# Performance work log

Hardware: AMD Instinct MI355X
Metric: run time of the kernel (lower is better)

Reference implementation:

```python
import jax, jax.numpy as jnp
import numpy as np

EPS = 1e-8
LN_EPS = 1e-5

def _layernorm(x, g, b):
    mu = jnp.mean(x, axis=-1, keepdims=True)
    var = jnp.mean((x - mu) ** 2, axis=-1, keepdims=True)
    return (x - mu) / jnp.sqrt(var + LN_EPS) * g + b

def setup_inputs() -> dict:
    key = jax.random.key(0)
    ks = jax.random.split(key, 10)
    B, S = 8192, 4096
    input_dim, hidden_dim = 4, 256
    h4 = hidden_dim // 4  # 64
    price_series = jax.random.uniform(ks[0], (B, S, 1), dtype=jnp.float32) + 0.5
    # 4 parallel encoders stacked on leading axis: Linear(input_dim->h4) + LayerNorm(h4)
    enc_w = jax.random.normal(ks[1], (4, input_dim, h4), dtype=jnp.float32) * 0.5
    enc_b = jax.random.normal(ks[2], (4, h4), dtype=jnp.float32) * 0.02
    enc_g = jnp.ones((4, h4), dtype=jnp.float32)
    enc_beta = jnp.zeros((4, h4), dtype=jnp.float32)
    # regime head: Linear(hidden_dim->64) + ReLU + (Dropout eval=identity) + Linear(64->4)
    head_w1 = jax.random.normal(ks[3], (hidden_dim, 64), dtype=jnp.float32) * 0.0625
    head_b1 = jnp.zeros((64,), dtype=jnp.float32)
    head_w2 = jax.random.normal(ks[4], (64, 4), dtype=jnp.float32) * 0.125
    head_b2 = jnp.zeros((4,), dtype=jnp.float32)
    return {"price_series": price_series, "enc_w": enc_w, "enc_b": enc_b,
            "enc_g": enc_g, "enc_beta": enc_beta,
            "head_w1": head_w1, "head_b1": head_b1,
            "head_w2": head_w2, "head_b2": head_b2}

def reference(price_series, enc_w, enc_b, enc_g, enc_beta, head_w1, head_b1, head_w2, head_b2):
    prices = price_series[:, :, 0]  # [B, S]
    B, S = prices.shape
    # Rolling SMA(20) with clamped window start, via cumsum (single pass, no per-step loop)
    csum = jnp.concatenate([jnp.zeros((B, 1), prices.dtype), jnp.cumsum(prices, axis=1)], axis=1)  # [B, S+1]
    i = jnp.arange(S)
    start20 = jnp.maximum(0, i - 19)
    cnt20 = (i - start20 + 1).astype(prices.dtype)
    sma20 = (csum[:, i + 1] - csum[:, start20]) / cnt20  # [B, S]
    trend_signal = (prices - sma20) / (sma20 + EPS)
    f_trend = jnp.mean(trend_signal, axis=1, keepdims=True)  # [B,1]
    # momentum over last 10 steps
    p_last = prices[:, -1:]
    p_m10 = prices[:, -10:-9]
    f_mom = (p_last - p_m10) / (p_m10 + EPS)  # [B,1]
    # mean reversion
    p_mean = jnp.mean(prices, axis=1, keepdims=True)
    f_mr = (p_last - p_mean) / (p_mean + EPS)  # [B,1]
    # cycle: coefficient of variation (torch.std is unbiased, ddof=1)
    f_cyc = jnp.std(prices, axis=1, ddof=1, keepdims=True) / (p_mean + EPS)  # [B,1]
    combined = jnp.concatenate([f_trend, f_mom, f_mr, f_cyc], axis=1)  # [B, 4]
    # 4 parallel encoders: Linear -> ReLU -> LayerNorm
    pre = jnp.einsum('bi,eio->ebo', combined, enc_w) + enc_b[:, None, :]  # [4, B, 64]
    feats = _layernorm(jax.nn.relu(pre), enc_g[:, None, :], enc_beta[:, None, :])  # [4, B, 64]
    # concat order: trend, momentum, mean_rev, cycle along feature dim
    regime_features = jnp.transpose(feats, (1, 0, 2)).reshape(B, -1)  # [B, 256]
    h = jax.nn.relu(regime_features @ head_w1 + head_b1)
    regime_probs = jax.nn.softmax(h @ head_w2 + head_b2, axis=1)  # [B, 4]
    return (regime_features, regime_probs)
```

## Files before the change

kernel.cpp:

```cpp
#include <hip/hip_runtime.h>

#define EPS 1e-8f
#define LN_EPS 1e-5f
#define NROWS 8192
#define SLEN 4096
#define PROBS_OFF 2097152

typedef __attribute__((ext_vector_type(8))) short bf16x8;
typedef __attribute__((ext_vector_type(4))) float f32x4;

__device__ __forceinline__ short f2bf(float f) {
    unsigned u = __float_as_uint(f);
    unsigned r = (u + 0x7FFFu + ((u >> 16) & 1u)) >> 16;
    return (short)r;
}

#define SLP(i) ((i) + ((((i) >> 4)) << 2))

__global__ __launch_bounds__(256) void k_feat(const float* __restrict__ prices,
                                              float* __restrict__ ws) {
    __shared__ float sld[5156];
    __shared__ float red[4][3];

    const int t = threadIdx.x;
    const int b = blockIdx.x;
    const int lane = t & 63, wv = t >> 6;
    const float4* R4 = (const float4*)(prices + (size_t)b * SLEN);

    if (t < 8) *(float4*)&sld[SLP(4 * t)] = make_float4(0.f, 0.f, 0.f, 0.f);
    {
        float4 g0 = R4[t];
        float4 g1 = R4[t + 256];
        float4 g2 = R4[t + 512];
        float4 g3 = R4[t + 768];
        *(float4*)&sld[SLP(4 * (t + 8))]   = g0;
        *(float4*)&sld[SLP(4 * (t + 264))] = g1;
        *(float4*)&sld[SLP(4 * (t + 520))] = g2;
        *(float4*)&sld[SLP(4 * (t + 776))] = g3;
    }
    __syncthreads();

    const int e0 = 16 * t + 32;
    float4 s0 = *(const float4*)&sld[SLP(e0)];
    float4 s1 = *(const float4*)&sld[SLP(e0 + 4)];
    float4 s2 = *(const float4*)&sld[SLP(e0 + 8)];
    float4 s3 = *(const float4*)&sld[SLP(e0 + 12)];
    float4 q0 = *(const float4*)&sld[SLP(e0 - 20)];
    float4 q1 = *(const float4*)&sld[SLP(e0 - 16)];
    float4 q2 = *(const float4*)&sld[SLP(e0 - 12)];
    float4 q3 = *(const float4*)&sld[SLP(e0 - 8)];
    float4 q4 = *(const float4*)&sld[SLP(e0 - 4)];

    float xv[16] = { s0.x, s0.y, s0.z, s0.w, s1.x, s1.y, s1.z, s1.w,
                     s2.x, s2.y, s2.z, s2.w, s3.x, s3.y, s3.z, s3.w };
    float ov[16] = { q0.x, q0.y, q0.z, q0.w, q1.x, q1.y, q1.z, q1.w,
                     q2.x, q2.y, q2.z, q2.w, q3.x, q3.y, q3.z, q3.w };

    float W = q0.y + q0.z + q0.w
            + q1.x + q1.y + q1.z + q1.w
            + q2.x + q2.y + q2.z + q2.w
            + q3.x + q3.y + q3.z + q3.w
            + q4.x + q4.y + q4.z + q4.w;

    const float pf = (float)(16 * t);
    float sum = 0.0f, sq = 0.0f, ts = 0.0f;
    #pragma unroll
    for (int j = 0; j < 16; ++j) {
        float x = xv[j];
        W += (j == 0) ? x : (x - ov[j]);
        sum += x;
        sq = fmaf(x, x, sq);
        float c = fminf(pf + (float)(j + 1), 20.0f);
        float num = fmaf(x, c, -W);
        float den = fmaf(EPS, c, W);
        ts += num * __builtin_amdgcn_rcpf(den);
    }

    #pragma unroll
    for (int off = 32; off > 0; off >>= 1) {
        sum += __shfl_xor(sum, off);
        sq  += __shfl_xor(sq,  off);
        ts  += __shfl_xor(ts,  off);
    }
    if (lane == 0) { red[wv][0] = sum; red[wv][1] = sq; red[wv][2] = ts; }
    __syncthreads();

    if (t == 255) {
        float S = red[0][0] + red[1][0] + red[2][0] + red[3][0];
        float Q = red[0][1] + red[1][1] + red[2][1] + red[3][1];
        float T = red[0][2] + red[1][2] + red[2][2] + red[3][2];
        float mean = S * (1.0f / 4096.0f);
        float var  = fmaxf((Q - 4096.0f * mean * mean) * (1.0f / 4095.0f), 0.0f);
        float p_m10 = s1.z, p_last = s3.w;
        float4 f;
        f.x = T * (1.0f / 4096.0f);
        f.y = (p_last - p_m10) / (p_m10 + EPS);
        f.z = (p_last - mean) / (mean + EPS);
        f.w = sqrtf(var) / (mean + EPS);
        ((float4*)ws)[b] = f;
    }
}

#define ROWS 16

__global__ __launch_bounds__(256) void k_head(
    const float* __restrict__ ws, float* __restrict__ out,
    const float* __restrict__ enc_w, const float* __restrict__ enc_b,
    const float* __restrict__ enc_g, const float* __restrict__ enc_bt,
    const float* __restrict__ w1, const float* __restrict__ b1,
    const float* __restrict__ w2, const float* __restrict__ b2)
{
    __shared__ float comb[ROWS][4];
    __shared__ short rfb[ROWS][264];
    __shared__ float hbuf[ROWS][68];

    const int t = threadIdx.x;
    const int r0 = blockIdx.x * ROWS;
    const int lane = t & 63, wave = t >> 6;
    const int l15 = lane & 15, q = lane >> 4;

    if (t < ROWS) *(float4*)comb[t] = ((const float4*)ws)[r0 + t];

    bf16x8 bfrag[8];
    #pragma unroll
    for (int kt = 0; kt < 8; ++kt) {
        #pragma unroll
        for (int j = 0; j < 8; ++j) {
            int k = kt * 32 + q * 8 + j;
            bfrag[kt][j] = f2bf(w1[k * 64 + wave * 16 + l15]);
        }
    }

    const float ew0 = enc_w[wave * 256 + lane];
    const float ew1v = enc_w[wave * 256 + 64 + lane];
    const float ew2v = enc_w[wave * 256 + 128 + lane];
    const float ew3v = enc_w[wave * 256 + 192 + lane];
    const float ebv = enc_b[t], egv = enc_g[t], btv = enc_bt[t];

    __syncthreads();

    for (int r = 0; r < ROWS; r += 2) {
        float4 cba = *(const float4*)comb[r];
        float4 cbb = *(const float4*)comb[r + 1];
        float va = fmaf(cba.x, ew0, fmaf(cba.y, ew1v, fmaf(cba.z, ew2v, fmaf(cba.w, ew3v, ebv))));
        float vb = fmaf(cbb.x, ew0, fmaf(cbb.y, ew1v, fmaf(cbb.z, ew2v, fmaf(cbb.w, ew3v, ebv))));
        va = fmaxf(va, 0.0f);
        vb = fmaxf(vb, 0.0f);
        float sma = va, smb = vb;
        #pragma unroll
        for (int off = 32; off > 0; off >>= 1) {
            sma += __shfl_xor(sma, off);
            smb += __shfl_xor(smb, off);
        }
        float mua = sma * (1.0f / 64.0f);
        float mub = smb * (1.0f / 64.0f);
        float da = va - mua, db = vb - mub;
        float vsa = da * da, vsb = db * db;
        #pragma unroll
        for (int off = 32; off > 0; off >>= 1) {
            vsa += __shfl_xor(vsa, off);
            vsb += __shfl_xor(vsb, off);
        }
        float ya = fmaf(da * rsqrtf(vsa * (1.0f / 64.0f) + LN_EPS), egv, btv);
        float yb = fmaf(db * rsqrtf(vsb * (1.0f / 64.0f) + LN_EPS), egv, btv);
        out[(size_t)(r0 + r) * 256 + t] = ya;
        out[(size_t)(r0 + r + 1) * 256 + t] = yb;
        rfb[r][t] = f2bf(ya);
        rfb[r + 1][t] = f2bf(yb);
    }
    __syncthreads();

    f32x4 acc0 = {0.f, 0.f, 0.f, 0.f};
    #pragma unroll
    for (int kt = 0; kt < 8; ++kt) {
        bf16x8 a0 = *(const bf16x8*)&rfb[l15][kt * 32 + q * 8];
        acc0 = __builtin_amdgcn_mfma_f32_16x16x32_bf16(a0, bfrag[kt], acc0, 0, 0, 0);
    }

    const int col = wave * 16 + l15;
    const float b1v = b1[col];
    #pragma unroll
    for (int rg = 0; rg < 4; ++rg)
        hbuf[q * 4 + rg][col] = fmaxf(acc0[rg] + b1v, 0.0f);
    __syncthreads();

    if (t < 4 * ROWS) {
        int r = t >> 2, c = t & 3;
        float a0 = 0.f, a1 = 0.f, a2 = 0.f, a3 = 0.f;
        #pragma unroll
        for (int j = 0; j < 16; ++j) {
            a0 = fmaf(hbuf[r][j],      w2[j * 4 + c],        a0);
            a1 = fmaf(hbuf[r][16 + j], w2[(16 + j) * 4 + c], a1);
            a2 = fmaf(hbuf[r][32 + j], w2[(32 + j) * 4 + c], a2);
            a3 = fmaf(hbuf[r][48 + j], w2[(48 + j) * 4 + c], a3);
        }
        float lg = b2[c] + ((a0 + a1) + (a2 + a3));
        float mx = fmaxf(lg, __shfl_xor(lg, 1, 4));
        mx = fmaxf(mx, __shfl_xor(mx, 2, 4));
        float ex = __expf(lg - mx);
        float s2 = ex + __shfl_xor(ex, 1, 4);
        s2 += __shfl_xor(s2, 2, 4);
        out[PROBS_OFF + (size_t)(r0 + r) * 4 + c] = ex / s2;
    }
}

extern "C" void kernel_launch(void* const* d_in, const int* in_sizes, int n_in,
                              void* d_out, int out_size, void* d_ws, size_t ws_size,
                              hipStream_t stream) {
    const float* prices  = (const float*)d_in[0];
    const float* enc_w   = (const float*)d_in[1];
    const float* enc_b   = (const float*)d_in[2];
    const float* enc_g   = (const float*)d_in[3];
    const float* enc_bt  = (const float*)d_in[4];
    const float* head_w1 = (const float*)d_in[5];
    const float* head_b1 = (const float*)d_in[6];
    const float* head_w2 = (const float*)d_in[7];
    const float* head_b2 = (const float*)d_in[8];
    float* out = (float*)d_out;
    float* ws  = (float*)d_ws;

    k_feat<<<NROWS, 256, 0, stream>>>(prices, ws);
    k_head<<<NROWS / ROWS, 256, 0, stream>>>(ws, out, enc_w, enc_b, enc_g, enc_bt,
                                             head_w1, head_b1, head_w2, head_b2);
}
```

Measured before the change: 212.4 us.

## Load price rows directly into LDS with XOR swizzle and specialize steady-state SMA loop

```diff
diff --git a/kernel.cpp b/kernel.cpp
--- a/kernel.cpp
+++ b/kernel.cpp
@@ -15,11 +15,18 @@
     return (short)r;
 }
 
-#define SLP(i) ((i) + ((((i) >> 4)) << 2))
+__device__ __forceinline__ void g2l16(const float4* g, float4* l) {
+    __builtin_amdgcn_global_load_lds(
+        (const __attribute__((address_space(1))) unsigned int*)g,
+        (__attribute__((address_space(3))) unsigned int*)l,
+        16, 0, 0);
+}
+
+__device__ __forceinline__ int swz(int s) { return s ^ ((s >> 3) & 7); }
 
 __global__ __launch_bounds__(256) void k_feat(const float* __restrict__ prices,
                                               float* __restrict__ ws) {
-    __shared__ float sld[5156];
+    __shared__ float4 sld4[1032];
     __shared__ float red[4][3];
 
     const int t = threadIdx.x;
@@ -27,29 +34,25 @@
     const int lane = t & 63, wv = t >> 6;
     const float4* R4 = (const float4*)(prices + (size_t)b * SLEN);
 
-    if (t < 8) *(float4*)&sld[SLP(4 * t)] = make_float4(0.f, 0.f, 0.f, 0.f);
-    {
-        float4 g0 = R4[t];
-        float4 g1 = R4[t + 256];
-        float4 g2 = R4[t + 512];
-        float4 g3 = R4[t + 768];
-        *(float4*)&sld[SLP(4 * (t + 8))]   = g0;
-        *(float4*)&sld[SLP(4 * (t + 264))] = g1;
-        *(float4*)&sld[SLP(4 * (t + 520))] = g2;
-        *(float4*)&sld[SLP(4 * (t + 776))] = g3;
-    }
-    __syncthreads();
-
-    const int e0 = 16 * t + 32;
-    float4 s0 = *(const float4*)&sld[SLP(e0)];
-    float4 s1 = *(const float4*)&sld[SLP(e0 + 4)];
-    float4 s2 = *(const float4*)&sld[SLP(e0 + 8)];
-    float4 s3 = *(const float4*)&sld[SLP(e0 + 12)];
-    float4 q0 = *(const float4*)&sld[SLP(e0 - 20)];
-    float4 q1 = *(const float4*)&sld[SLP(e0 - 16)];
-    float4 q2 = *(const float4*)&sld[SLP(e0 - 12)];
-    float4 q3 = *(const float4*)&sld[SLP(e0 - 8)];
-    float4 q4 = *(const float4*)&sld[SLP(e0 - 4)];
+    if (t < 8) sld4[t] = make_float4(0.f, 0.f, 0.f, 0.f);
+
+    #pragma unroll
+    for (int k = 0; k < 4; ++k) {
+        const int base = 8 + 256 * k + 64 * wv;
+        const int g = swz(base + lane) - 8;
+        g2l16(R4 + g, sld4 + base);
+    }
+    __syncthreads();
+
+    float4 q0 = sld4[swz(4 * t + 3)];
+    float4 q1 = sld4[swz(4 * t + 4)];
+    float4 q2 = sld4[swz(4 * t + 5)];
+    float4 q3 = sld4[swz(4 * t + 6)];
+    float4 q4 = sld4[swz(4 * t + 7)];
+    float4 s0 = sld4[swz(4 * t + 8)];
+    float4 s1 = sld4[swz(4 * t + 9)];
+    float4 s2 = sld4[swz(4 * t + 10)];
+    float4 s3 = sld4[swz(4 * t + 11)];
 
     float xv[16] = { s0.x, s0.y, s0.z, s0.w, s1.x, s1.y, s1.z, s1.w,
                      s2.x, s2.y, s2.z, s2.w, s3.x, s3.y, s3.z, s3.w };
@@ -62,18 +65,31 @@
             + q3.x + q3.y + q3.z + q3.w
             + q4.x + q4.y + q4.z + q4.w;
 
-    const float pf = (float)(16 * t);
     float sum = 0.0f, sq = 0.0f, ts = 0.0f;
-    #pragma unroll
-    for (int j = 0; j < 16; ++j) {
-        float x = xv[j];
-        W += (j == 0) ? x : (x - ov[j]);
-        sum += x;
-        sq = fmaf(x, x, sq);
-        float c = fminf(pf + (float)(j + 1), 20.0f);
-        float num = fmaf(x, c, -W);
-        float den = fmaf(EPS, c, W);
-        ts += num * __builtin_amdgcn_rcpf(den);
+    if (t >= 2) {
+        #pragma unroll
+        for (int j = 0; j < 16; ++j) {
+            float x = xv[j];
+            W += (j == 0) ? x : (x - ov[j]);
+            sum += x;
+            sq = fmaf(x, x, sq);
+            float num = fmaf(x, 20.0f, -W);
+            float den = W + (20.0f * EPS);
+            ts += num * __builtin_amdgcn_rcpf(den);
+        }
+    } else {
+        const float pf = (float)(16 * t);
+        #pragma unroll
+        for (int j = 0; j < 16; ++j) {
+            float x = xv[j];
+            W += (j == 0) ? x : (x - ov[j]);
+            sum += x;
+            sq = fmaf(x, x, sq);
+            float c = fminf(pf + (float)(j + 1), 20.0f);
+            float num = fmaf(x, c, -W);
+            float den = fmaf(EPS, c, W);
+            ts += num * __builtin_amdgcn_rcpf(den);
+        }
     }
 
     #pragma unroll
```

New measurement: 212.7 us. About the same (+0.1%).
